# Kernel tuning notes

Hardware: AMD Instinct MI355X
Metric: run time of the kernel (lower is better)

Reference implementation:

```python
import jax, jax.numpy as jnp
import numpy as np
from math import sqrt

B, T, D = 32, 65536, 512
NPOS, NTIME = 8192, 2048


def setup_inputs() -> dict:
    key = jax.random.key(0)
    rng = np.random.default_rng(0)
    # jagged lengths summing exactly to T
    raw = rng.integers(256, 4096, size=B).astype(np.float64)
    lengths = np.floor(raw / raw.sum() * T).astype(np.int64)
    lengths[-1] += T - lengths.sum()
    offsets = np.concatenate([[0], np.cumsum(lengths)]).astype(np.int64)
    # monotonically increasing timestamps (positive per-token deltas)
    deltas = rng.integers(1, 1000, size=T).astype(np.int64)
    timestamps = np.cumsum(deltas)
    # number of target items per sequence (strictly less than length)
    num_targets = np.minimum(rng.integers(0, 32, size=B), lengths // 2).astype(np.int64)
    k1, k2, k3 = jax.random.split(key, 3)
    seq_embeddings = jax.random.normal(k1, (T, D), dtype=jnp.float32)
    bp = sqrt(1.0 / NPOS)
    bt = sqrt(1.0 / NTIME)
    pos_emb = jax.random.uniform(k2, (NPOS, D), minval=-bp, maxval=bp, dtype=jnp.float32)
    ts_emb = jax.random.uniform(k3, (NTIME + 1, D), minval=-bt, maxval=bt, dtype=jnp.float32)
    return {
        "max_seq_len": 4096,
        "seq_lengths": jnp.asarray(lengths),
        "seq_offsets": jnp.asarray(offsets),
        "seq_embeddings": seq_embeddings,
        "num_targets": jnp.asarray(num_targets),
        "seq_timestamps": jnp.asarray(timestamps),
        "pos_emb": pos_emb,
        "ts_emb": ts_emb,
    }


def reference(max_seq_len, seq_lengths, seq_offsets, seq_embeddings, num_targets, seq_timestamps, pos_emb, ts_emb):
    T_, D_ = seq_embeddings.shape
    alpha = float(D_) ** 0.5
    max_pos_ind = pos_emb.shape[0]
    max_ts_ind = ts_emb.shape[0] - 1  # num_time_buckets

    tok = jnp.arange(T_)
    # sequence id per flat token via offsets (offsets[0]=0, offsets[B]=T)
    seq_id = jnp.searchsorted(seq_offsets, tok, side="right") - 1
    local = tok - seq_offsets[seq_id]                 # position within sequence
    L = seq_lengths[seq_id]

    # position bucket: targets share the position of the first target
    high = L - num_targets[seq_id]                    # interleave_targets=False
    high = jnp.minimum(high, max_pos_ind - 1)         # clamp to table size
    pos = jnp.clip(jnp.minimum(local, high), 0, max_pos_ind - 1)

    # time bucket: sqrt of delta to the sequence's last (query) timestamp
    query_ts = seq_timestamps[seq_offsets[seq_id] + L - 1]
    delta = jnp.maximum(query_ts - seq_timestamps, 0).astype(jnp.float32)
    bucket = jnp.floor(jnp.sqrt(delta)).astype(jnp.int32)
    bucket = jnp.clip(bucket, 0, max_ts_ind)

    # fused gather + scale + add
    return seq_embeddings * alpha + pos_emb[pos] + ts_emb[bucket]
```

## Files before the change

### kernel.cpp

```cpp
#include <hip/hip_runtime.h>
#include <math.h>

__global__ void hstu_meta_kernel(const int* __restrict__ seq_lengths,
                                 const int* __restrict__ seq_offsets,
                                 const int* __restrict__ num_targets,
                                 const int* __restrict__ seq_timestamps,
                                 int* __restrict__ pos_idx,
                                 int* __restrict__ bucket_idx,
                                 int T, int B, int NPOS, int NTIME) {
    int t = blockIdx.x * blockDim.x + threadIdx.x;
    if (t >= T) return;

    int lo = 0, hi = B;
    while (hi - lo > 1) {
        int mid = (lo + hi) >> 1;
        if (seq_offsets[mid] <= t) lo = mid; else hi = mid;
    }
    const int sid   = lo;
    const int off   = seq_offsets[sid];
    const int L     = seq_lengths[sid];
    const int local = t - off;

    int high = L - num_targets[sid];
    if (high > NPOS - 1) high = NPOS - 1;
    int pos = local < high ? local : high;
    if (pos < 0) pos = 0;
    if (pos > NPOS - 1) pos = NPOS - 1;

    const int qts   = seq_timestamps[off + L - 1];
    int delta = qts - seq_timestamps[t];
    if (delta < 0) delta = 0;
    int bucket = (int)floorf(sqrtf((float)delta));
    if (bucket < 0) bucket = 0;
    if (bucket > NTIME) bucket = NTIME;

    pos_idx[t]    = pos;
    bucket_idx[t] = bucket;
}

template <int C4_SHIFT>
__global__ void __launch_bounds__(256)
hstu_fuse_kernel_pow2(const float4* __restrict__ emb,
                      const float4* __restrict__ pos_emb,
                      const float4* __restrict__ ts_emb,
                      const int* __restrict__ pos_idx,
                      const int* __restrict__ bucket_idx,
                      float4* __restrict__ out,
                      int total4, float alpha) {
    const int stride = gridDim.x * blockDim.x;
    constexpr int C4 = 1 << C4_SHIFT;
    for (int idx = blockIdx.x * blockDim.x + threadIdx.x; idx < total4; idx += stride) {
        const int t = idx >> C4_SHIFT;
        const int c = idx & (C4 - 1);
        const int p = pos_idx[t];
        const int b = bucket_idx[t];
        const float4 e  = emb[idx];
        const float4 pe = pos_emb[(long)p * C4 + c];
        const float4 te = ts_emb[(long)b * C4 + c];
        float4 o;
        o.x = fmaf(e.x, alpha, pe.x + te.x);
        o.y = fmaf(e.y, alpha, pe.y + te.y);
        o.z = fmaf(e.z, alpha, pe.z + te.z);
        o.w = fmaf(e.w, alpha, pe.w + te.w);
        out[idx] = o;
    }
}

__global__ void __launch_bounds__(256)
hstu_fuse_kernel_gen(const float4* __restrict__ emb,
                     const float4* __restrict__ pos_emb,
                     const float4* __restrict__ ts_emb,
                     const int* __restrict__ pos_idx,
                     const int* __restrict__ bucket_idx,
                     float4* __restrict__ out,
                     int total4, int c4, float alpha) {
    const int stride = gridDim.x * blockDim.x;
    for (int idx = blockIdx.x * blockDim.x + threadIdx.x; idx < total4; idx += stride) {
        const int t = idx / c4;
        const int c = idx - t * c4;
        const int p = pos_idx[t];
        const int b = bucket_idx[t];
        const float4 e  = emb[idx];
        const float4 pe = pos_emb[(long)p * c4 + c];
        const float4 te = ts_emb[(long)b * c4 + c];
        float4 o;
        o.x = fmaf(e.x, alpha, pe.x + te.x);
        o.y = fmaf(e.y, alpha, pe.y + te.y);
        o.z = fmaf(e.z, alpha, pe.z + te.z);
        o.w = fmaf(e.w, alpha, pe.w + te.w);
        out[idx] = o;
    }
}

extern "C" void kernel_launch(void* const* d_in, const int* in_sizes, int n_in,
                              void* d_out, int out_size, void* d_ws, size_t ws_size,
                              hipStream_t stream) {
    const int* seq_lengths    = (const int*)d_in[1];
    const int* seq_offsets    = (const int*)d_in[2];
    const float* seq_emb      = (const float*)d_in[3];
    const int* num_targets    = (const int*)d_in[4];
    const int* seq_timestamps = (const int*)d_in[5];
    const float* pos_emb      = (const float*)d_in[6];
    const float* ts_emb       = (const float*)d_in[7];
    float* out                = (float*)d_out;

    const int B     = in_sizes[1];
    const int T     = in_sizes[5];
    const int D     = in_sizes[3] / T;
    const int NPOS  = in_sizes[6] / D;
    const int NTIME = in_sizes[7] / D - 1;
    const float alpha = sqrtf((float)D);

    int* pos_idx    = (int*)d_ws;
    int* bucket_idx = pos_idx + T;

    {
        const int block = 256;
        const int grid  = (T + block - 1) / block;
        hstu_meta_kernel<<<grid, block, 0, stream>>>(
            seq_lengths, seq_offsets, num_targets, seq_timestamps,
            pos_idx, bucket_idx, T, B, NPOS, NTIME);
    }

    {
        const int c4     = D / 4;
        const long total4l = (long)T * c4;
        const int total4 = (int)total4l;
        const int block  = 256;
        int grid = (int)((total4l + block - 1) / block);
        const int grid_cap = 256 * 8;
        if (grid > grid_cap) grid = grid_cap;

        if (c4 == 128) {
            hstu_fuse_kernel_pow2<7><<<grid, block, 0, stream>>>(
                (const float4*)seq_emb, (const float4*)pos_emb, (const float4*)ts_emb,
                pos_idx, bucket_idx, (float4*)out, total4, alpha);
        } else if (c4 == 64) {
            hstu_fuse_kernel_pow2<6><<<grid, block, 0, stream>>>(
                (const float4*)seq_emb, (const float4*)pos_emb, (const float4*)ts_emb,
                pos_idx, bucket_idx, (float4*)out, total4, alpha);
        } else if (c4 == 256) {
            hstu_fuse_kernel_pow2<8><<<grid, block, 0, stream>>>(
                (const float4*)seq_emb, (const float4*)pos_emb, (const float4*)ts_emb,
                pos_idx, bucket_idx, (float4*)out, total4, alpha);
        } else {
            hstu_fuse_kernel_gen<<<grid, block, 0, stream>>>(
                (const float4*)seq_emb, (const float4*)pos_emb, (const float4*)ts_emb,
                pos_idx, bucket_idx, (float4*)out, total4, c4, alpha);
        }
    }
}
```

Measured before the change: 266.3 us.

## Process one row per wavefront with packed meta and nontemporal streaming loads/stores

Packs the position and time-bucket indices into a single int2 per token and restructures the fused gather so that each 64-lane wavefront handles a whole row. Each lane loads two float4s per table, and the next row's metadata is prefetched while the current row is processed. The streaming embedding input and output use nontemporal loads and stores so they do not pollute the cache, leaving room for the reused pos/ts tables. This cuts per-element index math and index loads, at the cost of fewer threads in flight per row and a dependency on nontemporal hint behaviour.

```diff
diff --git a/kernel.cpp b/kernel.cpp
--- a/kernel.cpp
+++ b/kernel.cpp
@@ -1,12 +1,13 @@
 #include <hip/hip_runtime.h>
 #include <math.h>
+
+typedef float f32x4 __attribute__((ext_vector_type(4)));
 
 __global__ void hstu_meta_kernel(const int* __restrict__ seq_lengths,
                                  const int* __restrict__ seq_offsets,
                                  const int* __restrict__ num_targets,
                                  const int* __restrict__ seq_timestamps,
-                                 int* __restrict__ pos_idx,
-                                 int* __restrict__ bucket_idx,
+                                 int2* __restrict__ meta,
                                  int T, int B, int NPOS, int NTIME) {
     int t = blockIdx.x * blockDim.x + threadIdx.x;
     if (t >= T) return;
@@ -34,56 +35,78 @@
     if (bucket < 0) bucket = 0;
     if (bucket > NTIME) bucket = NTIME;
 
-    pos_idx[t]    = pos;
-    bucket_idx[t] = bucket;
+    meta[t] = make_int2(pos, bucket);
 }
 
-template <int C4_SHIFT>
+template <int C4S>
 __global__ void __launch_bounds__(256)
-hstu_fuse_kernel_pow2(const float4* __restrict__ emb,
-                      const float4* __restrict__ pos_emb,
-                      const float4* __restrict__ ts_emb,
-                      const int* __restrict__ pos_idx,
-                      const int* __restrict__ bucket_idx,
-                      float4* __restrict__ out,
-                      int total4, float alpha) {
-    const int stride = gridDim.x * blockDim.x;
-    constexpr int C4 = 1 << C4_SHIFT;
-    for (int idx = blockIdx.x * blockDim.x + threadIdx.x; idx < total4; idx += stride) {
-        const int t = idx >> C4_SHIFT;
-        const int c = idx & (C4 - 1);
-        const int p = pos_idx[t];
-        const int b = bucket_idx[t];
-        const float4 e  = emb[idx];
-        const float4 pe = pos_emb[(long)p * C4 + c];
-        const float4 te = ts_emb[(long)b * C4 + c];
-        float4 o;
-        o.x = fmaf(e.x, alpha, pe.x + te.x);
-        o.y = fmaf(e.y, alpha, pe.y + te.y);
-        o.z = fmaf(e.z, alpha, pe.z + te.z);
-        o.w = fmaf(e.w, alpha, pe.w + te.w);
-        out[idx] = o;
+hstu_fuse_wave_row(const f32x4* __restrict__ emb,
+                   const f32x4* __restrict__ pos_emb,
+                   const f32x4* __restrict__ ts_emb,
+                   const int2* __restrict__ meta,
+                   f32x4* __restrict__ out,
+                   int T, float alpha) {
+    constexpr int C4   = 1 << C4S;
+    constexpr int F4PL = C4 >> 6;
+    static_assert(F4PL >= 1, "row must span at least one float4 per lane");
+
+    const int lane = threadIdx.x & 63;
+    const int wpb  = blockDim.x >> 6;
+    const int nw   = gridDim.x * wpb;
+    int t = blockIdx.x * wpb + (threadIdx.x >> 6);
+    if (t >= T) return;
+
+    int2 m = meta[t];
+    while (true) {
+        const int tn = t + nw;
+        int2 mn = m;
+        if (tn < T) mn = meta[tn];
+
+        const f32x4* ep = emb     + (((size_t)t)   << C4S) + lane;
+        const f32x4* pp = pos_emb + (((size_t)m.x) << C4S) + lane;
+        const f32x4* tp = ts_emb  + (((size_t)m.y) << C4S) + lane;
+
+        f32x4 e[F4PL], p[F4PL], q[F4PL];
+#pragma unroll
+        for (int j = 0; j < F4PL; ++j) e[j] = __builtin_nontemporal_load(ep + 64 * j);
+#pragma unroll
+        for (int j = 0; j < F4PL; ++j) p[j] = pp[64 * j];
+#pragma unroll
+        for (int j = 0; j < F4PL; ++j) q[j] = tp[64 * j];
+
+        f32x4* op = out + (((size_t)t) << C4S) + lane;
+#pragma unroll
+        for (int j = 0; j < F4PL; ++j) {
+            f32x4 o;
+            o.x = fmaf(e[j].x, alpha, p[j].x + q[j].x);
+            o.y = fmaf(e[j].y, alpha, p[j].y + q[j].y);
+            o.z = fmaf(e[j].z, alpha, p[j].z + q[j].z);
+            o.w = fmaf(e[j].w, alpha, p[j].w + q[j].w);
+            __builtin_nontemporal_store(o, op + 64 * j);
+        }
+
+        if (tn >= T) break;
+        t = tn;
+        m = mn;
     }
 }
 
 __global__ void __launch_bounds__(256)
-hstu_fuse_kernel_gen(const float4* __restrict__ emb,
-                     const float4* __restrict__ pos_emb,
-                     const float4* __restrict__ ts_emb,
-                     const int* __restrict__ pos_idx,
-                     const int* __restrict__ bucket_idx,
-                     float4* __restrict__ out,
+hstu_fuse_kernel_gen(const f32x4* __restrict__ emb,
+                     const f32x4* __restrict__ pos_emb,
+                     const f32x4* __restrict__ ts_emb,
+                     const int2* __restrict__ meta,
+                     f32x4* __restrict__ out,
                      int total4, int c4, float alpha) {
     const int stride = gridDim.x * blockDim.x;
     for (int idx = blockIdx.x * blockDim.x + threadIdx.x; idx < total4; idx += stride) {
         const int t = idx / c4;
         const int c = idx - t * c4;
-        const int p = pos_idx[t];
-        const int b = bucket_idx[t];
-        const float4 e  = emb[idx];
-        const float4 pe = pos_emb[(long)p * c4 + c];
-        const float4 te = ts_emb[(long)b * c4 + c];
-        float4 o;
+        const int2 m = meta[t];
+        const f32x4 e  = emb[idx];
+        const f32x4 pe = pos_emb[(size_t)m.x * c4 + c];
+        const f32x4 te = ts_emb[(size_t)m.y * c4 + c];
+        f32x4 o;
         o.x = fmaf(e.x, alpha, pe.x + te.x);
         o.y = fmaf(e.y, alpha, pe.y + te.y);
         o.z = fmaf(e.z, alpha, pe.z + te.z);
@@ -111,42 +134,43 @@
     const int NTIME = in_sizes[7] / D - 1;
     const float alpha = sqrtf((float)D);
 
-    int* pos_idx    = (int*)d_ws;
-    int* bucket_idx = pos_idx + T;
+    int2* meta = (int2*)d_ws;
 
     {
         const int block = 256;
         const int grid  = (T + block - 1) / block;
         hstu_meta_kernel<<<grid, block, 0, stream>>>(
             seq_lengths, seq_offsets, num_targets, seq_timestamps,
-            pos_idx, bucket_idx, T, B, NPOS, NTIME);
+            meta, T, B, NPOS, NTIME);
     }
 
-    {
-        const int c4     = D / 4;
+    const int c4 = D / 4;
+    const int block = 256;
+    const int wpb = block / 64;
+
+    if (c4 == 128 || c4 == 64 || c4 == 256) {
+        int grid = (T + wpb - 1) / wpb;
+        if (grid > 2048) grid = 2048;
+        if (c4 == 128) {
+            hstu_fuse_wave_row<7><<<grid, block, 0, stream>>>(
+                (const f32x4*)seq_emb, (const f32x4*)pos_emb, (const f32x4*)ts_emb,
+                meta, (f32x4*)out, T, alpha);
+        } else if (c4 == 64) {
+            hstu_fuse_wave_row<6><<<grid, block, 0, stream>>>(
+                (const f32x4*)seq_emb, (const f32x4*)pos_emb, (const f32x4*)ts_emb,
+                meta, (f32x4*)out, T, alpha);
+        } else {
+            hstu_fuse_wave_row<8><<<grid, block, 0, stream>>>(
+                (const f32x4*)seq_emb, (const f32x4*)pos_emb, (const f32x4*)ts_emb,
+                meta, (f32x4*)out, T, alpha);
+        }
+    } else {
         const long total4l = (long)T * c4;
         const int total4 = (int)total4l;
-        const int block  = 256;
         int grid = (int)((total4l + block - 1) / block);
-        const int grid_cap = 256 * 8;
-        if (grid > grid_cap) grid = grid_cap;
-
-        if (c4 == 128) {
-            hstu_fuse_kernel_pow2<7><<<grid, block, 0, stream>>>(
-                (const float4*)seq_emb, (const float4*)pos_emb, (const float4*)ts_emb,
-                pos_idx, bucket_idx, (float4*)out, total4, alpha);
-        } else if (c4 == 64) {
-            hstu_fuse_kernel_pow2<6><<<grid, block, 0, stream>>>(
-                (const float4*)seq_emb, (const float4*)pos_emb, (const float4*)ts_emb,
-                pos_idx, bucket_idx, (float4*)out, total4, alpha);
-        } else if (c4 == 256) {
-            hstu_fuse_kernel_pow2<8><<<grid, block, 0, stream>>>(
-                (const float4*)seq_emb, (const float4*)pos_emb, (const float4*)ts_emb,
-                pos_idx, bucket_idx, (float4*)out, total4, alpha);
-        } else {
-            hstu_fuse_kernel_gen<<<grid, block, 0, stream>>>(
-                (const float4*)seq_emb, (const float4*)pos_emb, (const float4*)ts_emb,
-                pos_idx, bucket_idx, (float4*)out, total4, c4, alpha);
-        }
+        if (grid > 2048) grid = 2048;
+        hstu_fuse_kernel_gen<<<grid, block, 0, stream>>>(
+            (const f32x4*)seq_emb, (const f32x4*)pos_emb, (const f32x4*)ts_emb,
+            meta, (f32x4*)out, total4, c4, alpha);
     }
 }
```

After: 261.0 us. 1.02x faster.
